# Kernel tuning notes

Hardware: AMD Instinct MI355X
Metric: run time of the kernel (lower is better)

Reference implementation:

```python
import jax, jax.numpy as jnp
import numpy as np

B, NI, NN, E = 1024, 64, 8256, 131072  # batch, n_inputs, n_internal_neurons, n_edges
N_OUT = 64      # output neurons occupy internal indices [0, N_OUT)
N_PASSES = 2    # recurrent passes (activate(inputs, n_passes))


def setup_inputs() -> dict:
    key = jax.random.key(0)
    k1, k2, k3, k4, k5, k6 = jax.random.split(key, 6)
    inputs = jax.random.normal(k1, (B, NI), dtype=jnp.float32)
    # src index into concat([inputs, node_activs]) of width NI+NN;
    # src < NI means an input neuron (negative id in the original), else internal.
    src_idx = jax.random.randint(k2, (E,), 0, NI + NN, dtype=jnp.int32)
    dst_idx = jax.random.randint(k3, (E,), 0, NN, dtype=jnp.int32)
    weights = jax.random.normal(k4, (E,), dtype=jnp.float32) * 0.1
    bias = jax.random.normal(k5, (NN,), dtype=jnp.float32) * 0.1
    response = jax.random.uniform(k6, (NN,), dtype=jnp.float32, minval=0.5, maxval=1.5)
    return {"inputs": inputs, "weights": weights, "bias": bias,
            "response": response, "src_idx": src_idx, "dst_idx": dst_idx}


def reference(inputs, weights, bias, response, src_idx, dst_idx):
    # Neurons with no incoming connection must output exactly 0 (original code path).
    has_in = jnp.zeros((NN,), dtype=bool).at[dst_idx].set(True)

    def one_pass(state, _):
        # state: [B, NN] node activations from the previous pass
        vals = jnp.concatenate([inputs, state], axis=1)        # [B, NI+NN]
        msgs = vals[:, src_idx] * weights                      # [B, E] weighted incoming
        agg = jax.ops.segment_sum(msgs.T, dst_idx, num_segments=NN)  # [NN, B] sum-aggregation
        out = jnp.tanh(bias[:, None] + response[:, None] * agg).T    # [B, NN]
        out = jnp.where(has_in[None, :], out, jnp.zeros((), out.dtype))
        return out, None

    state0 = jnp.zeros((B, NN), dtype=inputs.dtype)
    state, _ = jax.lax.scan(one_pass, state0, None, length=N_PASSES)
    return state[:, :N_OUT]  # output neurons are the first N_OUT internal indices
```

## Files before the change

kernel.cpp:

```cpp
#include <hip/hip_runtime.h>

#define B       1024
#define NI      64
#define NN      8256
#define E_EDGES 131072
#define N_OUT   64

#define CAP1 16
#define CAP2 96

__global__ void init_kernel(int* __restrict__ hasIn, int* __restrict__ cntIn,
                            int* __restrict__ flags, int* __restrict__ cnt2) {
    int i = blockIdx.x * 256 + threadIdx.x;
    if (i < NN) { hasIn[i] = 0; cntIn[i] = 0; flags[i] = 0; }
    if (i < 64) cnt2[i] = 0;
}

__global__ void edges_kernel(const int* __restrict__ src, const int* __restrict__ dst,
                             const float* __restrict__ w,
                             int* __restrict__ hasIn,
                             int* __restrict__ cntIn, int* __restrict__ colIn, float* __restrict__ valIn,
                             int* __restrict__ flags,
                             int* __restrict__ cnt2, int* __restrict__ col2, float* __restrict__ val2) {
    int e = blockIdx.x * 256 + threadIdx.x;
    if (e >= E_EDGES) return;
    int s = src[e], d = dst[e];
    float wt = w[e];
    hasIn[d] = 1;
    if (s < NI) {
        int p = atomicAdd(&cntIn[d], 1);
        if (p < CAP1) { colIn[d * CAP1 + p] = s; valIn[d * CAP1 + p] = wt; }
    }
    if (d < 64) {
        int p = atomicAdd(&cnt2[d], 1);
        if (p < CAP2) { col2[d * CAP2 + p] = s; val2[d * CAP2 + p] = wt; }
        if (s >= NI) flags[s - NI] = 1;
    }
}

__global__ void transpose_in_kernel(const float* __restrict__ in, float* __restrict__ outT) {
    int tid = blockIdx.x * 256 + threadIdx.x;
    if (tid < NI * B) {
        int s = tid / B, b = tid % B;
        outT[tid] = in[b * NI + s];
    }
}

__global__ __launch_bounds__(256) void pass1_kernel(
    const float* __restrict__ inputsT,
    const int* __restrict__ flags,
    const int* __restrict__ hasIn,
    const int* __restrict__ cntIn, const int* __restrict__ colIn, const float* __restrict__ valIn,
    const float* __restrict__ bias, const float* __restrict__ response,
    float* __restrict__ state1T)
{
    int n = blockIdx.x;
    if (!flags[n]) return;
    int b = threadIdx.x * 4;
    float4 o = make_float4(0.f, 0.f, 0.f, 0.f);
    if (hasIn[n]) {
        int cnt = cntIn[n]; if (cnt > CAP1) cnt = CAP1;
        float4 acc = make_float4(0.f, 0.f, 0.f, 0.f);
        for (int e = 0; e < cnt; ++e) {
            int s = colIn[n * CAP1 + e];
            float wt = valIn[n * CAP1 + e];
            float4 v = *(const float4*)(inputsT + (size_t)s * B + b);
            acc.x = fmaf(wt, v.x, acc.x);
            acc.y = fmaf(wt, v.y, acc.y);
            acc.z = fmaf(wt, v.z, acc.z);
            acc.w = fmaf(wt, v.w, acc.w);
        }
        float bi = bias[n], rr = response[n];
        o.x = tanhf(fmaf(rr, acc.x, bi));
        o.y = tanhf(fmaf(rr, acc.y, bi));
        o.z = tanhf(fmaf(rr, acc.z, bi));
        o.w = tanhf(fmaf(rr, acc.w, bi));
    }
    *(float4*)(state1T + (size_t)n * B + b) = o;
}

__global__ __launch_bounds__(256) void pass2_kernel(
    const float* __restrict__ inputsT,
    const float* __restrict__ state1T,
    const int* __restrict__ hasIn,
    const int* __restrict__ cnt2, const int* __restrict__ col2, const float* __restrict__ val2,
    const float* __restrict__ bias, const float* __restrict__ response,
    float* __restrict__ state2T)
{
    int n = blockIdx.x;
    int b = threadIdx.x * 4;
    float4 o = make_float4(0.f, 0.f, 0.f, 0.f);
    if (hasIn[n]) {
        int cnt = cnt2[n]; if (cnt > CAP2) cnt = CAP2;
        float4 acc = make_float4(0.f, 0.f, 0.f, 0.f);
        for (int e = 0; e < cnt; ++e) {
            int s = col2[n * CAP2 + e];
            float wt = val2[n * CAP2 + e];
            const float* row = (s < NI) ? (inputsT + (size_t)s * B)
                                        : (state1T + (size_t)(s - NI) * B);
            float4 v = *(const float4*)(row + b);
            acc.x = fmaf(wt, v.x, acc.x);
            acc.y = fmaf(wt, v.y, acc.y);
            acc.z = fmaf(wt, v.z, acc.z);
            acc.w = fmaf(wt, v.w, acc.w);
        }
        float bi = bias[n], rr = response[n];
        o.x = tanhf(fmaf(rr, acc.x, bi));
        o.y = tanhf(fmaf(rr, acc.y, bi));
        o.z = tanhf(fmaf(rr, acc.z, bi));
        o.w = tanhf(fmaf(rr, acc.w, bi));
    }
    *(float4*)(state2T + (size_t)n * B + b) = o;
}

__global__ void gather_kernel(const float* __restrict__ state2T, float* __restrict__ out) {
    int tid = blockIdx.x * 256 + threadIdx.x;
    if (tid < B * N_OUT) {
        int b = tid / N_OUT, n = tid % N_OUT;
        out[tid] = state2T[(size_t)n * B + b];
    }
}

extern "C" void kernel_launch(void* const* d_in, const int* in_sizes, int n_in,
                              void* d_out, int out_size, void* d_ws, size_t ws_size,
                              hipStream_t stream) {
    const float* inputs   = (const float*)d_in[0];
    const float* weights  = (const float*)d_in[1];
    const float* bias     = (const float*)d_in[2];
    const float* response = (const float*)d_in[3];
    const int*   src_idx  = (const int*)d_in[4];
    const int*   dst_idx  = (const int*)d_in[5];
    float* out = (float*)d_out;

    char* ws = (char*)d_ws;
    size_t off = 0;
    auto alloc = [&](size_t bytes) -> void* {
        void* p = ws + off;
        off = (off + bytes + 255) & ~(size_t)255;
        return p;
    };
    float* inputsT = (float*)alloc((size_t)NI * B * sizeof(float));
    float* state1T = (float*)alloc((size_t)NN * B * sizeof(float));
    float* state2T = (float*)alloc((size_t)N_OUT * B * sizeof(float));
    int*   hasIn   = (int*)alloc(NN * sizeof(int));
    int*   cntIn   = (int*)alloc(NN * sizeof(int));
    int*   flags   = (int*)alloc(NN * sizeof(int));
    int*   cnt2    = (int*)alloc(64 * sizeof(int));
    int*   colIn   = (int*)alloc((size_t)NN * CAP1 * sizeof(int));
    float* valIn   = (float*)alloc((size_t)NN * CAP1 * sizeof(float));
    int*   col2    = (int*)alloc((size_t)64 * CAP2 * sizeof(int));
    float* val2    = (float*)alloc((size_t)64 * CAP2 * sizeof(float));

    init_kernel<<<(NN + 255) / 256, 256, 0, stream>>>(hasIn, cntIn, flags, cnt2);
    edges_kernel<<<E_EDGES / 256, 256, 0, stream>>>(src_idx, dst_idx, weights,
                                                    hasIn, cntIn, colIn, valIn,
                                                    flags, cnt2, col2, val2);
    transpose_in_kernel<<<(NI * B) / 256, 256, 0, stream>>>(inputs, inputsT);
    pass1_kernel<<<NN, 256, 0, stream>>>(inputsT, flags, hasIn, cntIn, colIn, valIn,
                                         bias, response, state1T);
    pass2_kernel<<<64, 256, 0, stream>>>(inputsT, state1T, hasIn, cnt2, col2, val2,
                                         bias, response, state2T);
    gather_kernel<<<(B * N_OUT) / 256, 256, 0, stream>>>(state2T, out);
}
```

Baseline: 90.10 us.

## Fuse all stages into one cooperative kernel with grid syncs and a worklist

Replaces the six separate launches (init, edge scan, input transpose, pass 1, pass 2, gather) with one cooperative kernel of 512 blocks. Grid-wide syncs separate the stages. The edge scan now builds a compacted worklist of the internal neurons that feed the outputs, so pass 1 loops only over those instead of launching 8256 blocks that mostly exit early. Pass 2 writes straight into the output layout, which drops the state2T buffer and the gather kernel. The cost is three grid syncs, and the kernel depends on all 512 blocks being co-resident and on the worklist fitting in its fixed capacity.

Result: slower. 252.1 us (+179.8%).

```diff
diff --git a/kernel.cpp b/kernel.cpp
--- a/kernel.cpp
+++ b/kernel.cpp
@@ -1,4 +1,7 @@
 #include <hip/hip_runtime.h>
+#include <hip/hip_cooperative_groups.h>
+
+namespace cg = cooperative_groups;
 
 #define B       1024
 #define NI      64
@@ -6,118 +9,124 @@
 #define E_EDGES 131072
 #define N_OUT   64
 
-#define CAP1 16
-#define CAP2 96
+#define CAP1    16
+#define CAP2    96
+#define WCAP    4096
+#define GRID    512
+#define TPB     256
 
-__global__ void init_kernel(int* __restrict__ hasIn, int* __restrict__ cntIn,
-                            int* __restrict__ flags, int* __restrict__ cnt2) {
-    int i = blockIdx.x * 256 + threadIdx.x;
-    if (i < NN) { hasIn[i] = 0; cntIn[i] = 0; flags[i] = 0; }
-    if (i < 64) cnt2[i] = 0;
-}
+__global__ __launch_bounds__(TPB, 4) void mega_kernel(
+    const float* __restrict__ inputs,
+    const float* __restrict__ weights,
+    const float* __restrict__ bias,
+    const float* __restrict__ response,
+    const int* __restrict__ src,
+    const int* __restrict__ dst,
+    float* __restrict__ out,
+    float* __restrict__ inputsT,
+    float* __restrict__ state1T,
+    int* __restrict__ hasIn,
+    int* __restrict__ cntIn,
+    int* __restrict__ colIn,
+    float* __restrict__ valIn,
+    int* __restrict__ flags,
+    int* __restrict__ cnt2,
+    int* __restrict__ col2,
+    float* __restrict__ val2,
+    int* __restrict__ worklist,
+    int* __restrict__ nWork)
+{
+    cg::grid_group grid = cg::this_grid();
+    const int tid = blockIdx.x * TPB + threadIdx.x;
 
-__global__ void edges_kernel(const int* __restrict__ src, const int* __restrict__ dst,
-                             const float* __restrict__ w,
-                             int* __restrict__ hasIn,
-                             int* __restrict__ cntIn, int* __restrict__ colIn, float* __restrict__ valIn,
-                             int* __restrict__ flags,
-                             int* __restrict__ cnt2, int* __restrict__ col2, float* __restrict__ val2) {
-    int e = blockIdx.x * 256 + threadIdx.x;
-    if (e >= E_EDGES) return;
-    int s = src[e], d = dst[e];
-    float wt = w[e];
-    hasIn[d] = 1;
-    if (s < NI) {
-        int p = atomicAdd(&cntIn[d], 1);
-        if (p < CAP1) { colIn[d * CAP1 + p] = s; valIn[d * CAP1 + p] = wt; }
-    }
-    if (d < 64) {
-        int p = atomicAdd(&cnt2[d], 1);
-        if (p < CAP2) { col2[d * CAP2 + p] = s; val2[d * CAP2 + p] = wt; }
-        if (s >= NI) flags[s - NI] = 1;
-    }
-}
-
-__global__ void transpose_in_kernel(const float* __restrict__ in, float* __restrict__ outT) {
-    int tid = blockIdx.x * 256 + threadIdx.x;
+    if (tid < NN) { hasIn[tid] = 0; cntIn[tid] = 0; flags[tid] = 0; }
+    if (tid < 64) cnt2[tid] = 0;
+    if (tid == 0) *nWork = 0;
     if (tid < NI * B) {
         int s = tid / B, b = tid % B;
-        outT[tid] = in[b * NI + s];
+        inputsT[tid] = inputs[b * NI + s];
     }
-}
+    grid.sync();
 
-__global__ __launch_bounds__(256) void pass1_kernel(
-    const float* __restrict__ inputsT,
-    const int* __restrict__ flags,
-    const int* __restrict__ hasIn,
-    const int* __restrict__ cntIn, const int* __restrict__ colIn, const float* __restrict__ valIn,
-    const float* __restrict__ bias, const float* __restrict__ response,
-    float* __restrict__ state1T)
-{
-    int n = blockIdx.x;
-    if (!flags[n]) return;
-    int b = threadIdx.x * 4;
-    float4 o = make_float4(0.f, 0.f, 0.f, 0.f);
-    if (hasIn[n]) {
-        int cnt = cntIn[n]; if (cnt > CAP1) cnt = CAP1;
-        float4 acc = make_float4(0.f, 0.f, 0.f, 0.f);
-        for (int e = 0; e < cnt; ++e) {
-            int s = colIn[n * CAP1 + e];
-            float wt = valIn[n * CAP1 + e];
-            float4 v = *(const float4*)(inputsT + (size_t)s * B + b);
-            acc.x = fmaf(wt, v.x, acc.x);
-            acc.y = fmaf(wt, v.y, acc.y);
-            acc.z = fmaf(wt, v.z, acc.z);
-            acc.w = fmaf(wt, v.w, acc.w);
+    if (tid < E_EDGES) {
+        int s = src[tid], d = dst[tid];
+        float wt = weights[tid];
+        hasIn[d] = 1;
+        if (s < NI) {
+            int p = atomicAdd(&cntIn[d], 1);
+            if (p < CAP1) { colIn[d * CAP1 + p] = s; valIn[d * CAP1 + p] = wt; }
         }
-        float bi = bias[n], rr = response[n];
-        o.x = tanhf(fmaf(rr, acc.x, bi));
-        o.y = tanhf(fmaf(rr, acc.y, bi));
-        o.z = tanhf(fmaf(rr, acc.z, bi));
-        o.w = tanhf(fmaf(rr, acc.w, bi));
+        if (d < 64) {
+            int p = atomicAdd(&cnt2[d], 1);
+            if (p < CAP2) { col2[d * CAP2 + p] = s; val2[d * CAP2 + p] = wt; }
+            if (s >= NI) {
+                int n = s - NI;
+                if (atomicExch(&flags[n], 1) == 0) {
+                    int q = atomicAdd(nWork, 1);
+                    if (q < WCAP) worklist[q] = n;
+                }
+            }
+        }
     }
-    *(float4*)(state1T + (size_t)n * B + b) = o;
-}
+    grid.sync();
 
-__global__ __launch_bounds__(256) void pass2_kernel(
-    const float* __restrict__ inputsT,
-    const float* __restrict__ state1T,
-    const int* __restrict__ hasIn,
-    const int* __restrict__ cnt2, const int* __restrict__ col2, const float* __restrict__ val2,
-    const float* __restrict__ bias, const float* __restrict__ response,
-    float* __restrict__ state2T)
-{
-    int n = blockIdx.x;
-    int b = threadIdx.x * 4;
-    float4 o = make_float4(0.f, 0.f, 0.f, 0.f);
-    if (hasIn[n]) {
-        int cnt = cnt2[n]; if (cnt > CAP2) cnt = CAP2;
-        float4 acc = make_float4(0.f, 0.f, 0.f, 0.f);
-        for (int e = 0; e < cnt; ++e) {
-            int s = col2[n * CAP2 + e];
-            float wt = val2[n * CAP2 + e];
-            const float* row = (s < NI) ? (inputsT + (size_t)s * B)
-                                        : (state1T + (size_t)(s - NI) * B);
-            float4 v = *(const float4*)(row + b);
-            acc.x = fmaf(wt, v.x, acc.x);
-            acc.y = fmaf(wt, v.y, acc.y);
-            acc.z = fmaf(wt, v.z, acc.z);
-            acc.w = fmaf(wt, v.w, acc.w);
+    {
+        int nw = *nWork; if (nw > WCAP) nw = WCAP;
+        int b = threadIdx.x * 4;
+        for (int w = blockIdx.x; w < nw; w += gridDim.x) {
+            int n = worklist[w];
+            float4 o = make_float4(0.f, 0.f, 0.f, 0.f);
+            if (hasIn[n]) {
+                int cnt = cntIn[n]; if (cnt > CAP1) cnt = CAP1;
+                float4 acc = make_float4(0.f, 0.f, 0.f, 0.f);
+                for (int e = 0; e < cnt; ++e) {
+                    int s = colIn[n * CAP1 + e];
+                    float wt = valIn[n * CAP1 + e];
+                    float4 v = *(const float4*)(inputsT + (size_t)s * B + b);
+                    acc.x = fmaf(wt, v.x, acc.x);
+                    acc.y = fmaf(wt, v.y, acc.y);
+                    acc.z = fmaf(wt, v.z, acc.z);
+                    acc.w = fmaf(wt, v.w, acc.w);
+                }
+                float bi = bias[n], rr = response[n];
+                o.x = tanhf(fmaf(rr, acc.x, bi));
+                o.y = tanhf(fmaf(rr, acc.y, bi));
+                o.z = tanhf(fmaf(rr, acc.z, bi));
+                o.w = tanhf(fmaf(rr, acc.w, bi));
+            }
+            *(float4*)(state1T + (size_t)n * B + b) = o;
         }
-        float bi = bias[n], rr = response[n];
-        o.x = tanhf(fmaf(rr, acc.x, bi));
-        o.y = tanhf(fmaf(rr, acc.y, bi));
-        o.z = tanhf(fmaf(rr, acc.z, bi));
-        o.w = tanhf(fmaf(rr, acc.w, bi));
     }
-    *(float4*)(state2T + (size_t)n * B + b) = o;
-}
+    grid.sync();
 
-__global__ void gather_kernel(const float* __restrict__ state2T, float* __restrict__ out) {
-    int tid = blockIdx.x * 256 + threadIdx.x;
-    if (tid < B * N_OUT) {
-        int b = tid / N_OUT, n = tid % N_OUT;
-        out[tid] = state2T[(size_t)n * B + b];
+    if (blockIdx.x < N_OUT) {
+        int n = blockIdx.x;
+        int b = threadIdx.x * 4;
+        float4 o = make_float4(0.f, 0.f, 0.f, 0.f);
+        if (hasIn[n]) {
+            int cnt = cnt2[n]; if (cnt > CAP2) cnt = CAP2;
+            float4 acc = make_float4(0.f, 0.f, 0.f, 0.f);
+            for (int e = 0; e < cnt; ++e) {
+                int s = col2[n * CAP2 + e];
+                float wt = val2[n * CAP2 + e];
+                const float* row = (s < NI) ? (inputsT + (size_t)s * B)
+                                            : (state1T + (size_t)(s - NI) * B);
+                float4 v = *(const float4*)(row + b);
+                acc.x = fmaf(wt, v.x, acc.x);
+                acc.y = fmaf(wt, v.y, acc.y);
+                acc.z = fmaf(wt, v.z, acc.z);
+                acc.w = fmaf(wt, v.w, acc.w);
+            }
+            float bi = bias[n], rr = response[n];
+            o.x = tanhf(fmaf(rr, acc.x, bi));
+            o.y = tanhf(fmaf(rr, acc.y, bi));
+            o.z = tanhf(fmaf(rr, acc.z, bi));
+            o.w = tanhf(fmaf(rr, acc.w, bi));
+        }
+        out[(size_t)(b + 0) * N_OUT + n] = o.x;
+        out[(size_t)(b + 1) * N_OUT + n] = o.y;
+        out[(size_t)(b + 2) * N_OUT + n] = o.z;
+        out[(size_t)(b + 3) * N_OUT + n] = o.w;
     }
 }
 
@@ -139,26 +148,27 @@
         off = (off + bytes + 255) & ~(size_t)255;
         return p;
     };
-    float* inputsT = (float*)alloc((size_t)NI * B * sizeof(float));
-    float* state1T = (float*)alloc((size_t)NN * B * sizeof(float));
-    float* state2T = (float*)alloc((size_t)N_OUT * B * sizeof(float));
-    int*   hasIn   = (int*)alloc(NN * sizeof(int));
-    int*   cntIn   = (int*)alloc(NN * sizeof(int));
-    int*   flags   = (int*)alloc(NN * sizeof(int));
-    int*   cnt2    = (int*)alloc(64 * sizeof(int));
-    int*   colIn   = (int*)alloc((size_t)NN * CAP1 * sizeof(int));
-    float* valIn   = (float*)alloc((size_t)NN * CAP1 * sizeof(float));
-    int*   col2    = (int*)alloc((size_t)64 * CAP2 * sizeof(int));
-    float* val2    = (float*)alloc((size_t)64 * CAP2 * sizeof(float));
+    float* inputsT  = (float*)alloc((size_t)NI * B * sizeof(float));
+    float* state1T  = (float*)alloc((size_t)NN * B * sizeof(float));
+    int*   hasIn    = (int*)alloc(NN * sizeof(int));
+    int*   cntIn    = (int*)alloc(NN * sizeof(int));
+    int*   flags    = (int*)alloc(NN * sizeof(int));
+    int*   cnt2     = (int*)alloc(64 * sizeof(int));
+    int*   colIn    = (int*)alloc((size_t)NN * CAP1 * sizeof(int));
+    float* valIn    = (float*)alloc((size_t)NN * CAP1 * sizeof(float));
+    int*   col2     = (int*)alloc((size_t)64 * CAP2 * sizeof(int));
+    float* val2     = (float*)alloc((size_t)64 * CAP2 * sizeof(float));
+    int*   worklist = (int*)alloc(WCAP * sizeof(int));
+    int*   nWork    = (int*)alloc(sizeof(int));
 
-    init_kernel<<<(NN + 255) / 256, 256, 0, stream>>>(hasIn, cntIn, flags, cnt2);
-    edges_kernel<<<E_EDGES / 256, 256, 0, stream>>>(src_idx, dst_idx, weights,
-                                                    hasIn, cntIn, colIn, valIn,
-                                                    flags, cnt2, col2, val2);
-    transpose_in_kernel<<<(NI * B) / 256, 256, 0, stream>>>(inputs, inputsT);
-    pass1_kernel<<<NN, 256, 0, stream>>>(inputsT, flags, hasIn, cntIn, colIn, valIn,
-                                         bias, response, state1T);
-    pass2_kernel<<<64, 256, 0, stream>>>(inputsT, state1T, hasIn, cnt2, col2, val2,
-                                         bias, response, state2T);
-    gather_kernel<<<(B * N_OUT) / 256, 256, 0, stream>>>(state2T, out);
+    void* args[] = {
+        (void*)&inputs, (void*)&weights, (void*)&bias, (void*)&response,
+        (void*)&src_idx, (void*)&dst_idx, (void*)&out,
+        (void*)&inputsT, (void*)&state1T,
+        (void*)&hasIn, (void*)&cntIn, (void*)&colIn, (void*)&valIn,
+        (void*)&flags, (void*)&cnt2, (void*)&col2, (void*)&val2,
+        (void*)&worklist, (void*)&nWork
+    };
+    hipLaunchCooperativeKernel((void*)mega_kernel, dim3(GRID), dim3(TPB),
+                               args, 0, stream);
 }
```

## Fuse pass1 into pass2 by recomputing needed first-pass activations on the fly

Applied to the files above, without the earlier changes.

Pass 1 is no longer materialised for flagged neurons. The output kernel now recomputes each needed first-pass activation inline from the input-edge lists, writes straight to the output layout, and drops the gather kernel. The input transpose is merged into the init kernel, cutting the launch count from six to three and removing the state1T write and read traffic. The cost is redundant recomputation when many output neurons share sources, scalar per-thread loads in place of float4, and only 256 blocks in the final kernel.

Result: slower. 96.30 us (+6.9%).

```diff
diff --git a/kernel.cpp b/kernel.cpp
--- a/kernel.cpp
+++ b/kernel.cpp
@@ -6,22 +6,26 @@
 #define E_EDGES 131072
 #define N_OUT   64
 
-#define CAP1 16
-#define CAP2 96
+#define CAP1    16
+#define CAP2    96
 
-__global__ void init_kernel(int* __restrict__ hasIn, int* __restrict__ cntIn,
-                            int* __restrict__ flags, int* __restrict__ cnt2) {
-    int i = blockIdx.x * 256 + threadIdx.x;
-    if (i < NN) { hasIn[i] = 0; cntIn[i] = 0; flags[i] = 0; }
-    if (i < 64) cnt2[i] = 0;
+__global__ __launch_bounds__(256) void init_kernel(
+    const float* __restrict__ inputs,
+    float* __restrict__ inputsT,
+    int* __restrict__ hasIn, int* __restrict__ cntIn, int* __restrict__ cnt2) {
+    int tid = blockIdx.x * 256 + threadIdx.x;
+    if (tid < NN) { hasIn[tid] = 0; cntIn[tid] = 0; }
+    if (tid < 64) cnt2[tid] = 0;
+    int s = tid >> 10, b = tid & 1023;
+    inputsT[tid] = inputs[b * NI + s];
 }
 
-__global__ void edges_kernel(const int* __restrict__ src, const int* __restrict__ dst,
-                             const float* __restrict__ w,
-                             int* __restrict__ hasIn,
-                             int* __restrict__ cntIn, int* __restrict__ colIn, float* __restrict__ valIn,
-                             int* __restrict__ flags,
-                             int* __restrict__ cnt2, int* __restrict__ col2, float* __restrict__ val2) {
+__global__ __launch_bounds__(256) void edges_kernel(
+    const int* __restrict__ src, const int* __restrict__ dst,
+    const float* __restrict__ w,
+    int* __restrict__ hasIn,
+    int* __restrict__ cntIn, int* __restrict__ colIn, float* __restrict__ valIn,
+    int* __restrict__ cnt2, int* __restrict__ col2, float* __restrict__ val2) {
     int e = blockIdx.x * 256 + threadIdx.x;
     if (e >= E_EDGES) return;
     int s = src[e], d = dst[e];
@@ -34,91 +38,47 @@
     if (d < 64) {
         int p = atomicAdd(&cnt2[d], 1);
         if (p < CAP2) { col2[d * CAP2 + p] = s; val2[d * CAP2 + p] = wt; }
-        if (s >= NI) flags[s - NI] = 1;
     }
 }
 
-__global__ void transpose_in_kernel(const float* __restrict__ in, float* __restrict__ outT) {
-    int tid = blockIdx.x * 256 + threadIdx.x;
-    if (tid < NI * B) {
-        int s = tid / B, b = tid % B;
-        outT[tid] = in[b * NI + s];
-    }
-}
-
-__global__ __launch_bounds__(256) void pass1_kernel(
+__global__ __launch_bounds__(256) void out_kernel(
     const float* __restrict__ inputsT,
-    const int* __restrict__ flags,
     const int* __restrict__ hasIn,
     const int* __restrict__ cntIn, const int* __restrict__ colIn, const float* __restrict__ valIn,
-    const float* __restrict__ bias, const float* __restrict__ response,
-    float* __restrict__ state1T)
-{
-    int n = blockIdx.x;
-    if (!flags[n]) return;
-    int b = threadIdx.x * 4;
-    float4 o = make_float4(0.f, 0.f, 0.f, 0.f);
-    if (hasIn[n]) {
-        int cnt = cntIn[n]; if (cnt > CAP1) cnt = CAP1;
-        float4 acc = make_float4(0.f, 0.f, 0.f, 0.f);
-        for (int e = 0; e < cnt; ++e) {
-            int s = colIn[n * CAP1 + e];
-            float wt = valIn[n * CAP1 + e];
-            float4 v = *(const float4*)(inputsT + (size_t)s * B + b);
-            acc.x = fmaf(wt, v.x, acc.x);
-            acc.y = fmaf(wt, v.y, acc.y);
-            acc.z = fmaf(wt, v.z, acc.z);
-            acc.w = fmaf(wt, v.w, acc.w);
-        }
-        float bi = bias[n], rr = response[n];
-        o.x = tanhf(fmaf(rr, acc.x, bi));
-        o.y = tanhf(fmaf(rr, acc.y, bi));
-        o.z = tanhf(fmaf(rr, acc.z, bi));
-        o.w = tanhf(fmaf(rr, acc.w, bi));
-    }
-    *(float4*)(state1T + (size_t)n * B + b) = o;
-}
-
-__global__ __launch_bounds__(256) void pass2_kernel(
-    const float* __restrict__ inputsT,
-    const float* __restrict__ state1T,
-    const int* __restrict__ hasIn,
     const int* __restrict__ cnt2, const int* __restrict__ col2, const float* __restrict__ val2,
     const float* __restrict__ bias, const float* __restrict__ response,
-    float* __restrict__ state2T)
+    float* __restrict__ out)
 {
-    int n = blockIdx.x;
-    int b = threadIdx.x * 4;
-    float4 o = make_float4(0.f, 0.f, 0.f, 0.f);
+    int n = blockIdx.x & 63;
+    int b = ((blockIdx.x >> 6) << 8) + threadIdx.x;
+    float o = 0.f;
     if (hasIn[n]) {
         int cnt = cnt2[n]; if (cnt > CAP2) cnt = CAP2;
-        float4 acc = make_float4(0.f, 0.f, 0.f, 0.f);
+        float acc = 0.f;
         for (int e = 0; e < cnt; ++e) {
             int s = col2[n * CAP2 + e];
             float wt = val2[n * CAP2 + e];
-            const float* row = (s < NI) ? (inputsT + (size_t)s * B)
-                                        : (state1T + (size_t)(s - NI) * B);
-            float4 v = *(const float4*)(row + b);
-            acc.x = fmaf(wt, v.x, acc.x);
-            acc.y = fmaf(wt, v.y, acc.y);
-            acc.z = fmaf(wt, v.z, acc.z);
-            acc.w = fmaf(wt, v.w, acc.w);
+            float v;
+            if (s < NI) {
+                v = inputsT[s * B + b];
+            } else {
+                int m = s - NI;
+                v = 0.f;
+                if (hasIn[m]) {
+                    int c1 = cntIn[m]; if (c1 > CAP1) c1 = CAP1;
+                    float a1 = 0.f;
+                    for (int j = 0; j < c1; ++j) {
+                        int sj = colIn[m * CAP1 + j];
+                        a1 = fmaf(valIn[m * CAP1 + j], inputsT[sj * B + b], a1);
+                    }
+                    v = tanhf(fmaf(response[m], a1, bias[m]));
+                }
+            }
+            o = fmaf(wt, v, o);
         }
-        float bi = bias[n], rr = response[n];
-        o.x = tanhf(fmaf(rr, acc.x, bi));
-        o.y = tanhf(fmaf(rr, acc.y, bi));
-        o.z = tanhf(fmaf(rr, acc.z, bi));
-        o.w = tanhf(fmaf(rr, acc.w, bi));
+        o = tanhf(fmaf(response[n], o, bias[n]));
     }
-    *(float4*)(state2T + (size_t)n * B + b) = o;
-}
-
-__global__ void gather_kernel(const float* __restrict__ state2T, float* __restrict__ out) {
-    int tid = blockIdx.x * 256 + threadIdx.x;
-    if (tid < B * N_OUT) {
-        int b = tid / N_OUT, n = tid % N_OUT;
-        out[tid] = state2T[(size_t)n * B + b];
-    }
+    out[(size_t)b * N_OUT + n] = o;
 }
 
 extern "C" void kernel_launch(void* const* d_in, const int* in_sizes, int n_in,
@@ -140,25 +100,18 @@
         return p;
     };
     float* inputsT = (float*)alloc((size_t)NI * B * sizeof(float));
-    float* state1T = (float*)alloc((size_t)NN * B * sizeof(float));
-    float* state2T = (float*)alloc((size_t)N_OUT * B * sizeof(float));
     int*   hasIn   = (int*)alloc(NN * sizeof(int));
     int*   cntIn   = (int*)alloc(NN * sizeof(int));
-    int*   flags   = (int*)alloc(NN * sizeof(int));
     int*   cnt2    = (int*)alloc(64 * sizeof(int));
     int*   colIn   = (int*)alloc((size_t)NN * CAP1 * sizeof(int));
     float* valIn   = (float*)alloc((size_t)NN * CAP1 * sizeof(float));
     int*   col2    = (int*)alloc((size_t)64 * CAP2 * sizeof(int));
     float* val2    = (float*)alloc((size_t)64 * CAP2 * sizeof(float));
 
-    init_kernel<<<(NN + 255) / 256, 256, 0, stream>>>(hasIn, cntIn, flags, cnt2);
+    init_kernel<<<(NI * B) / 256, 256, 0, stream>>>(inputs, inputsT, hasIn, cntIn, cnt2);
     edges_kernel<<<E_EDGES / 256, 256, 0, stream>>>(src_idx, dst_idx, weights,
                                                     hasIn, cntIn, colIn, valIn,
-                                                    flags, cnt2, col2, val2);
-    transpose_in_kernel<<<(NI * B) / 256, 256, 0, stream>>>(inputs, inputsT);
-    pass1_kernel<<<NN, 256, 0, stream>>>(inputsT, flags, hasIn, cntIn, colIn, valIn,
-                                         bias, response, state1T);
-    pass2_kernel<<<64, 256, 0, stream>>>(inputsT, state1T, hasIn, cnt2, col2, val2,
-                                         bias, response, state2T);
-    gather_kernel<<<(B * N_OUT) / 256, 256, 0, stream>>>(state2T, out);
+                                                    cnt2, col2, val2);
+    out_kernel<<<256, 256, 0, stream>>>(inputsT, hasIn, cntIn, colIn, valIn,
+                                        cnt2, col2, val2, bias, response, out);
 }
```
